# Kernel tuning notes

Hardware: AMD Instinct MI355X
Metric: run time of the kernel (lower is better)

## Reference

```python
import jax, jax.numpy as jnp
import numpy as np

N, L, D, H = 2, 2048, 1024, 16
DK = D // H  # 64


def setup_inputs() -> dict:
    key = jax.random.key(0)
    ks = jax.random.split(key, 8)
    Xq = jax.random.normal(ks[0], (N, L, D), dtype=jnp.float32)
    Xk = jax.random.normal(ks[1], (N, L, D), dtype=jnp.float32)
    Xv = jax.random.normal(ks[2], (N, L, D), dtype=jnp.float32)
    mask_2d = jax.random.randint(ks[3], (N, L, L), 0, 2, dtype=jnp.int32)
    scale = 0.02
    Wq = jax.random.normal(ks[4], (D, D), dtype=jnp.float32) * scale
    Wk = jax.random.normal(ks[5], (D, D), dtype=jnp.float32) * scale
    Wv = jax.random.normal(ks[6], (D, D), dtype=jnp.float32) * scale
    Wo = jax.random.normal(ks[7], (D, D), dtype=jnp.float32) * scale
    return {"Xq": Xq, "Xk": Xk, "Xv": Xv, "Wq": Wq, "Wk": Wk, "Wv": Wv, "Wo": Wo, "mask_2d": mask_2d}


def reference(Xq, Xk, Xv, Wq, Wk, Wv, Wo, mask_2d):
    # Projections (bias=False). Per-head slicing in the original == reshape to [N,L,H,DK].
    Q = (Xq @ Wq).reshape(N, L, H, DK)
    K = (Xk @ Wk).reshape(N, L, H, DK)
    V = (Xv @ Wv).reshape(N, L, H, DK)
    # Scaled dot-product scores: [N, H, L, L]
    scores = jnp.einsum("blhd,bmhd->bhlm", Q, K) / jnp.sqrt(jnp.asarray(DK, scores_dtype(Q)))
    # NOTE: original uses masked_fill(mask==0, 0) BEFORE softmax (zero-fill, not -inf).
    scores = jnp.where(mask_2d[:, None, :, :] == 0, jnp.zeros((), scores.dtype), scores)
    A = jax.nn.softmax(scores, axis=-1)
    O = jnp.einsum("bhlm,bmhd->blhd", A, V).reshape(N, L, D)
    return O @ Wo


def scores_dtype(Q):
    return Q.dtype
```

## Files before the change

kernel.cpp:

```cpp
#include <hip/hip_runtime.h>
#include <hip/hip_bf16.h>

#define NB 2
#define L_SEQ 2048
#define NH 16
#define DKH 64
#define DMODEL 1024
#define MROWS (NB * L_SEQ)
#define QSCALE 0.18033688f

typedef __attribute__((ext_vector_type(8))) short short8;
typedef __attribute__((ext_vector_type(4))) float f32x4;

static __device__ __forceinline__ unsigned short f2bf(float f) {
    unsigned u = __float_as_uint(f);
    u += 0x7fffu + ((u >> 16) & 1u);
    return (unsigned short)(u >> 16);
}

static __device__ __forceinline__ float fexp2(float x) {
#if __has_builtin(__builtin_amdgcn_exp2f)
    return __builtin_amdgcn_exp2f(x);
#else
    return __expf(x * 0.6931471806f);
#endif
}

static __device__ __forceinline__ unsigned pk_bf16(float a, float b) {
    __hip_bfloat162 h = __float22bfloat162_rn(make_float2(a, b));
    return *reinterpret_cast<unsigned*>(&h);
}

static __device__ __forceinline__ void gll16(const void* g, void* l) {
    __builtin_amdgcn_global_load_lds(
        (const __attribute__((address_space(1))) void*)g,
        (__attribute__((address_space(3))) void*)l, 16, 0, 0);
}

__global__ __launch_bounds__(256)
void cast3(const float* __restrict__ s0, const float* __restrict__ s1,
           const float* __restrict__ s2, unsigned short* __restrict__ dst)
{
    const int z = blockIdx.z;
    const float* src = (z == 0) ? s0 : (z == 1) ? s1 : s2;
    const size_t i4 = (size_t)blockIdx.x * 256 + threadIdx.x;
    float4 v = ((const float4*)src)[i4];
    ushort4 o;
    o.x = f2bf(v.x); o.y = f2bf(v.y); o.z = f2bf(v.z); o.w = f2bf(v.w);
    ((ushort4*)(dst + (size_t)z * 4194304))[i4] = o;
}

__global__ __launch_bounds__(256)
void castWt(const float* __restrict__ w0, const float* __restrict__ w1,
            const float* __restrict__ w2, const float* __restrict__ w3,
            unsigned short* __restrict__ dst)
{
    __shared__ float ts[32][33];
    const int z = blockIdx.z;
    const float* W = (z == 0) ? w0 : (z == 1) ? w1 : (z == 2) ? w2 : w3;
    unsigned short* Wt = dst + (size_t)z * 1048576;

    const int k0 = blockIdx.y * 32;
    const int n0 = blockIdx.x * 32;
    const int t  = threadIdx.x;
    const int r  = t >> 3;
    const int c  = (t & 7) * 4;

    float4 v = *(const float4*)&W[(size_t)(k0 + r) * DMODEL + n0 + c];
    ts[r][c + 0] = v.x; ts[r][c + 1] = v.y; ts[r][c + 2] = v.z; ts[r][c + 3] = v.w;
    __syncthreads();

    ushort4 o;
    o.x = f2bf(ts[c + 0][r]); o.y = f2bf(ts[c + 1][r]);
    o.z = f2bf(ts[c + 2][r]); o.w = f2bf(ts[c + 3][r]);
    *(ushort4*)&Wt[(size_t)(n0 + r) * DMODEL + k0 + c] = o;
}

__global__ __launch_bounds__(256)
void maskbits(const int* __restrict__ mask, unsigned long long* __restrict__ MWT)
{
    const int lane = threadIdx.x & 63;
    const size_t wid = (size_t)blockIdx.x * 4 + (threadIdx.x >> 6);
    const int mv = mask[wid * 64 + lane];
    const unsigned long long bits = __ballot(mv != 0);
    if (lane == 0) {
        const int b   = (int)(wid >> 16);
        const int rem = (int)(wid & 65535);
        const int row = rem >> 5;
        const int wd  = rem & 31;
        MWT[((size_t)b * 32 + wd) * L_SEQ + row] = bits;
    }
}

__global__ __launch_bounds__(256)
void gemm_bf16(const unsigned short* __restrict__ Aall,
               const unsigned short* __restrict__ Ball,
               void* __restrict__ Oall,
               const int out_mode, const size_t a_zs, const size_t b_zs,
               const size_t o_zs)
{
    __shared__ __align__(16) unsigned short SMEM[16384];
    unsigned short* As = SMEM;
    unsigned short* Bs = SMEM + 8192;

    const int t    = threadIdx.x;
    const int w    = t >> 6;
    const int lane = t & 63;
    const int z    = blockIdx.z;
    const int m0   = blockIdx.y * 128;
    const int n0   = blockIdx.x * 128;

    const unsigned short* A = Aall + (size_t)z * a_zs;
    const unsigned short* B = Ball + (size_t)z * b_zs;

    const int srow = lane >> 3;
    const int sc   = (lane & 7) ^ srow;

    const unsigned short* ag[4];
    const unsigned short* bg[4];
    unsigned short* la[4];
    unsigned short* lb[4];
#pragma unroll
    for (int j = 0; j < 4; ++j) {
        const int R = w * 32 + j * 8;
        ag[j] = A + (size_t)(m0 + R + srow) * DMODEL + sc * 8;
        bg[j] = B + (size_t)(n0 + R + srow) * DMODEL + sc * 8;
        la[j] = As + R * 64;
        lb[j] = Bs + R * 64;
    }

    const int ml = lane & 15;
    const int q  = lane >> 4;
    const int wm = (w >> 1) * 64;
    const int wn = (w & 1) * 64;

    const f32x4 z4 = {0.f, 0.f, 0.f, 0.f};
    f32x4 acc[4][4];
#pragma unroll
    for (int i = 0; i < 4; ++i)
#pragma unroll
        for (int j = 0; j < 4; ++j) acc[i][j] = z4;

    for (int kt = 0; kt < DMODEL; kt += 64) {
        __syncthreads();
#pragma unroll
        for (int j = 0; j < 4; ++j) {
            gll16(ag[j] + kt, la[j]);
            gll16(bg[j] + kt, lb[j]);
        }
        __syncthreads();

#pragma unroll
        for (int s = 0; s < 2; ++s) {
            short8 av[4], bv[4];
#pragma unroll
            for (int mt = 0; mt < 4; ++mt)
                av[mt] = *(const short8*)
                    &As[(wm + mt * 16 + ml) * 64 + (((s * 4 + q) ^ (ml & 7)) * 8)];
#pragma unroll
            for (int nt = 0; nt < 4; ++nt)
                bv[nt] = *(const short8*)
                    &Bs[(wn + nt * 16 + ml) * 64 + (((s * 4 + q) ^ (ml & 7)) * 8)];
#pragma unroll
            for (int mt = 0; mt < 4; ++mt)
#pragma unroll
                for (int nt = 0; nt < 4; ++nt)
                    acc[mt][nt] = __builtin_amdgcn_mfma_f32_16x16x32_bf16(
                        av[mt], bv[nt], acc[mt][nt], 0, 0, 0);
        }
    }

    if (out_mode == 0) {
        unsigned short* O = (unsigned short*)Oall + (size_t)z * o_zs;
        if (z == 2) {
            __syncthreads();
            unsigned short* Ts = SMEM;
#pragma unroll
            for (int mt = 0; mt < 4; ++mt) {
                const int trow0 = wm + mt * 16 + q * 4;
                const int ch    = trow0 >> 3;
#pragma unroll
                for (int nt = 0; nt < 4; ++nt) {
                    const int tcol = wn + nt * 16 + ml;
                    const int pc   = (ch & 8) | ((ch & 7) ^ (tcol & 7));
                    ushort4 pv;
                    pv.x = f2bf(acc[mt][nt][0]); pv.y = f2bf(acc[mt][nt][1]);
                    pv.z = f2bf(acc[mt][nt][2]); pv.w = f2bf(acc[mt][nt][3]);
                    *(ushort4*)&Ts[tcol * 128 + pc * 8 + (trow0 & 7)] = pv;
                }
            }
            __syncthreads();
            const int bb = m0 >> 11;
            const int l0 = (m0 & (L_SEQ - 1)) + (t & 15) * 8;
            const int cr = t & 15;
#pragma unroll
            for (int it = 0; it < 8; ++it) {
                const int tcol = (t >> 4) + 16 * it;
                const int pc   = (cr & 8) | ((cr & 7) ^ (tcol & 7));
                short8 vv = *(const short8*)&Ts[tcol * 128 + pc * 8];
                const int n  = n0 + tcol;
                const int hh = n >> 6;
                const int dk = n & (DKH - 1);
                *(short8*)&O[((size_t)(bb * NH + hh) * DKH + dk) * L_SEQ + l0] = vv;
            }
        } else {
            const float qs = (z == 0) ? QSCALE : 1.0f;
#pragma unroll
            for (int mt = 0; mt < 4; ++mt) {
                const int gr0 = m0 + wm + mt * 16 + q * 4;
#pragma unroll
                for (int nt = 0; nt < 4; ++nt) {
                    const int col = n0 + wn + nt * 16 + ml;
                    const int hh  = col >> 6;
                    const int dk  = col & (DKH - 1);
#pragma unroll
                    for (int r = 0; r < 4; ++r) {
                        const int row = gr0 + r;
                        const int bb  = row >> 11;
                        const int l   = row & (L_SEQ - 1);
                        O[(((size_t)(bb * NH + hh) * L_SEQ + l) << 6) + dk] =
                            f2bf(acc[mt][nt][r] * qs);
                    }
                }
            }
        }
    } else {
        float* O = (float*)Oall;
#pragma unroll
        for (int mt = 0; mt < 4; ++mt) {
            const int gr0 = m0 + wm + mt * 16 + q * 4;
#pragma unroll
            for (int nt = 0; nt < 4; ++nt) {
                const int col = n0 + wn + nt * 16 + ml;
#pragma unroll
                for (int r = 0; r < 4; ++r)
                    O[(size_t)(gr0 + r) * DMODEL + col] = acc[mt][nt][r];
            }
        }
    }
}

__global__ __launch_bounds__(256, 4)
void attn_mfma(const unsigned short* __restrict__ Qb,
               const unsigned short* __restrict__ Kb,
               const unsigned short* __restrict__ Vtb,
               const unsigned long long* __restrict__ MWT,
               unsigned short* __restrict__ OB)
{
    __shared__ __align__(16) unsigned short Qs[64 * 64];
    __shared__ __align__(16) unsigned short Ks[64 * 64];
    __shared__ __align__(16) unsigned short Vts[64 * 64];
    __shared__ __align__(16) unsigned short Ps[4][16 * 64];
    __shared__ __align__(16) unsigned long long MskL[64];

    const int t    = threadIdx.x;
    const int w    = t >> 6;
    const int lane = t & 63;
    const int ml   = lane & 15;
    const int quad = lane >> 4;

    const int bid = blockIdx.x;
    const int p   = (bid >> 8) * 8 + (bid & 7);
    const int jq  = (bid >> 3) & 31;
    const int h   = p & 15;
    const int b   = p >> 4;
    const int q0  = jq * 64;

    const size_t hoff = (size_t)(b * NH + h) * L_SEQ * DKH;
    const unsigned short* Qh  = Qb  + hoff;
    const unsigned short* Kh  = Kb  + hoff;
    const unsigned short* Vth = Vtb + hoff;

    const int srow = lane >> 3;
    const int sc   = (lane & 7) ^ srow;

    gll16(Qh + (size_t)(q0 + w * 16 + srow) * DKH + sc * 8, &Qs[(w * 16) * 64]);
    gll16(Qh + (size_t)(q0 + w * 16 + 8 + srow) * DKH + sc * 8, &Qs[(w * 16 + 8) * 64]);
    __syncthreads();

    short8 qf[2];
#pragma unroll
    for (int s = 0; s < 2; ++s)
        qf[s] = *(const short8*)
            &Qs[(w * 16 + ml) * 64 + (((s * 4 + quad) ^ (ml & 7)) * 8)];

    const unsigned short* kg0 = Kh + (size_t)(w * 16 + srow) * DKH + sc * 8;
    const unsigned short* kg1 = Kh + (size_t)(w * 16 + 8 + srow) * DKH + sc * 8;
    const unsigned short* vg0 = Vth + (size_t)(w * 16 + srow) * L_SEQ + sc * 8;
    const unsigned short* vg1 = Vth + (size_t)(w * 16 + 8 + srow) * L_SEQ + sc * 8;
    unsigned short* lk0 = &Ks[(w * 16) * 64];
    unsigned short* lk1 = &Ks[(w * 16 + 8) * 64];
    unsigned short* lv0 = &Vts[(w * 16) * 64];
    unsigned short* lv1 = &Vts[(w * 16 + 8) * 64];

    const unsigned long long* mg = MWT + (size_t)b * 32 * L_SEQ + q0 + t;
    unsigned long long m_pf = 0;
    if (t < 64) m_pf = mg[0];

    f32x4 oacc[4];
    const f32x4 z4 = {0.f, 0.f, 0.f, 0.f};
#pragma unroll
    for (int dt = 0; dt < 4; ++dt) oacc[dt] = z4;
    float l_i = 0.f;

    for (int j = 0; j < 32; ++j) {
        __syncthreads();
        gll16(kg0, lk0);  gll16(kg1, lk1);
        gll16(vg0, lv0);  gll16(vg1, lv1);
        kg0 += 64 * DKH;  kg1 += 64 * DKH;
        vg0 += 64;        vg1 += 64;
        if (t < 64) {
            MskL[t] = m_pf;
            if (j < 31) m_pf = mg[(size_t)(j + 1) * L_SEQ];
        }
        __syncthreads();

        f32x4 sacc[4];
#pragma unroll
        for (int kt = 0; kt < 4; ++kt) sacc[kt] = z4;
#pragma unroll
        for (int s = 0; s < 2; ++s) {
            short8 kf[4];
#pragma unroll
            for (int kt = 0; kt < 4; ++kt)
                kf[kt] = *(const short8*)
                    &Ks[(kt * 16 + ml) * 64 + (((s * 4 + quad) ^ (ml & 7)) * 8)];
#pragma unroll
            for (int kt = 0; kt < 4; ++kt)
                sacc[kt] = __builtin_amdgcn_mfma_f32_16x16x32_bf16(
                    kf[kt], qf[s], sacc[kt], 0, 0, 0);
        }

        const unsigned long long wq = MskL[w * 16 + ml] >> (quad * 4);
        const unsigned mlo = (unsigned)wq;
        const unsigned mhi = (unsigned)(wq >> 32);
        float rs = 0.f;
        float pr[4][4];
#pragma unroll
        for (int kt = 0; kt < 4; ++kt) {
            const unsigned word = (kt < 2) ? mlo : mhi;
            const int base = (kt & 1) * 16;
#pragma unroll
            for (int r = 0; r < 4; ++r) {
                const float mf = (float)((word >> (base + r)) & 1u);
                const float e  = fexp2(sacc[kt][r] * mf);
                pr[kt][r] = e;
                rs += e;
            }
        }
        rs += __shfl_xor(rs, 16);
        rs += __shfl_xor(rs, 32);
        l_i += rs;
#pragma unroll
        for (int kt = 0; kt < 4; ++kt) {
            uint2 pk;
            pk.x = pk_bf16(pr[kt][0], pr[kt][1]);
            pk.y = pk_bf16(pr[kt][2], pr[kt][3]);
            const int cp = (kt * 2 + (quad >> 1)) ^ (ml & 7);
            *(uint2*)&Ps[w][ml * 64 + cp * 8 + (quad & 1) * 4] = pk;
        }

#pragma unroll
        for (int s = 0; s < 2; ++s) {
            const short8 pf = *(const short8*)
                &Ps[w][ml * 64 + (((s * 4 + quad) ^ (ml & 7)) * 8)];
#pragma unroll
            for (int dt = 0; dt < 4; ++dt) {
                const short8 vf = *(const short8*)
                    &Vts[(dt * 16 + ml) * 64 + (((s * 4 + quad) ^ (ml & 7)) * 8)];
                oacc[dt] = __builtin_amdgcn_mfma_f32_16x16x32_bf16(
                    vf, pf, oacc[dt], 0, 0, 0);
            }
        }
    }

    const float inv = 1.0f / l_i;
    const int qrow = q0 + w * 16 + ml;
#pragma unroll
    for (int dt = 0; dt < 4; ++dt) {
        ushort4 o4;
        o4.x = f2bf(oacc[dt][0] * inv);
        o4.y = f2bf(oacc[dt][1] * inv);
        o4.z = f2bf(oacc[dt][2] * inv);
        o4.w = f2bf(oacc[dt][3] * inv);
        *(ushort4*)&OB[(size_t)(b * L_SEQ + qrow) * DMODEL + h * DKH +
                       dt * 16 + quad * 4] = o4;
    }
}

extern "C" void kernel_launch(void* const* d_in, const int* in_sizes, int n_in,
                              void* d_out, int out_size, void* d_ws, size_t ws_size,
                              hipStream_t stream)
{
    (void)in_sizes; (void)n_in; (void)out_size; (void)ws_size;

    const float* Xq   = (const float*)d_in[0];
    const float* Xk   = (const float*)d_in[1];
    const float* Xv   = (const float*)d_in[2];
    const float* Wq   = (const float*)d_in[3];
    const float* Wk   = (const float*)d_in[4];
    const float* Wv   = (const float*)d_in[5];
    const float* Wo   = (const float*)d_in[6];
    const int*   mask = (const int*)d_in[7];
    float* out = (float*)d_out;

    char* base = (char*)d_ws;
    unsigned short*     XB  = (unsigned short*)base;
    unsigned short*     WtB = (unsigned short*)(base + (24u << 20));
    unsigned short*     QKV = (unsigned short*)(base + (32u << 20));
    unsigned short*     OB  = (unsigned short*)(base + (56u << 20));
    unsigned long long* MWT = (unsigned long long*)(base + (64u << 20));

    const size_t tsz = (size_t)MROWS * DMODEL;

    cast3<<<dim3(4096, 1, 3), 256, 0, stream>>>(Xq, Xk, Xv, XB);
    castWt<<<dim3(32, 32, 4), 256, 0, stream>>>(Wq, Wk, Wv, Wo, WtB);
    maskbits<<<dim3(32768), 256, 0, stream>>>(mask, MWT);

    gemm_bf16<<<dim3(8, 32, 3), 256, 0, stream>>>(
        XB, WtB, (void*)QKV, 0, tsz, (size_t)DMODEL * DMODEL, tsz);

    attn_mfma<<<dim3(1024), 256, 0, stream>>>(
        QKV, QKV + tsz, QKV + 2 * tsz, MWT, OB);

    gemm_bf16<<<dim3(8, 32, 1), 256, 0, stream>>>(
        OB, WtB + 3 * (size_t)DMODEL * DMODEL, (void*)out, 1, 0, 0, 0);
}
```

Measured before the change: 271.5 us.

## Merge prep kernels, double-buffer GEMM and attention loads, retile output GEMM

```diff
diff --git a/kernel.cpp b/kernel.cpp
--- a/kernel.cpp
+++ b/kernel.cpp
@@ -8,6 +8,7 @@
 #define DMODEL 1024
 #define MROWS (NB * L_SEQ)
 #define QSCALE 0.18033688f
+#define DD (DMODEL * DMODEL)
 
 typedef __attribute__((ext_vector_type(8))) short short8;
 typedef __attribute__((ext_vector_type(4))) float f32x4;
@@ -38,70 +39,64 @@
 }
 
 __global__ __launch_bounds__(256)
-void cast3(const float* __restrict__ s0, const float* __restrict__ s1,
-           const float* __restrict__ s2, unsigned short* __restrict__ dst)
-{
-    const int z = blockIdx.z;
-    const float* src = (z == 0) ? s0 : (z == 1) ? s1 : s2;
-    const size_t i4 = (size_t)blockIdx.x * 256 + threadIdx.x;
-    float4 v = ((const float4*)src)[i4];
-    ushort4 o;
-    o.x = f2bf(v.x); o.y = f2bf(v.y); o.z = f2bf(v.z); o.w = f2bf(v.w);
-    ((ushort4*)(dst + (size_t)z * 4194304))[i4] = o;
-}
-
-__global__ __launch_bounds__(256)
-void castWt(const float* __restrict__ w0, const float* __restrict__ w1,
-            const float* __restrict__ w2, const float* __restrict__ w3,
-            unsigned short* __restrict__ dst)
+void prep(const float* __restrict__ Xq, const float* __restrict__ Xk,
+          const float* __restrict__ Xv, const float* __restrict__ w0,
+          const float* __restrict__ w1, const float* __restrict__ w2,
+          const float* __restrict__ w3, const int* __restrict__ mask,
+          unsigned short* __restrict__ XB, unsigned short* __restrict__ WtB,
+          unsigned long long* __restrict__ MWT)
 {
     __shared__ float ts[32][33];
-    const int z = blockIdx.z;
-    const float* W = (z == 0) ? w0 : (z == 1) ? w1 : (z == 2) ? w2 : w3;
-    unsigned short* Wt = dst + (size_t)z * 1048576;
-
-    const int k0 = blockIdx.y * 32;
-    const int n0 = blockIdx.x * 32;
+    const int bx = blockIdx.x;
     const int t  = threadIdx.x;
-    const int r  = t >> 3;
-    const int c  = (t & 7) * 4;
-
-    float4 v = *(const float4*)&W[(size_t)(k0 + r) * DMODEL + n0 + c];
-    ts[r][c + 0] = v.x; ts[r][c + 1] = v.y; ts[r][c + 2] = v.z; ts[r][c + 3] = v.w;
-    __syncthreads();
-
-    ushort4 o;
-    o.x = f2bf(ts[c + 0][r]); o.y = f2bf(ts[c + 1][r]);
-    o.z = f2bf(ts[c + 2][r]); o.w = f2bf(ts[c + 3][r]);
-    *(ushort4*)&Wt[(size_t)(n0 + r) * DMODEL + k0 + c] = o;
+
+    if (bx < 12288) {
+        const int z = bx >> 12;
+        const float* src = (z == 0) ? Xq : (z == 1) ? Xk : Xv;
+        const size_t i4 = (size_t)(bx & 4095) * 256 + t;
+        float4 v = ((const float4*)src)[i4];
+        ushort4 o;
+        o.x = f2bf(v.x); o.y = f2bf(v.y); o.z = f2bf(v.z); o.w = f2bf(v.w);
+        ((ushort4*)(XB + (size_t)z * 4194304))[i4] = o;
+    } else if (bx < 16384) {
+        const int idx = bx - 12288;
+        const int z   = idx >> 10;
+        const int rem = idx & 1023;
+        const float* W = (z == 0) ? w0 : (z == 1) ? w1 : (z == 2) ? w2 : w3;
+        unsigned short* Wt = WtB + (size_t)z * DD;
+        const int n0 = (rem & 31) * 32;
+        const int k0 = (rem >> 5) * 32;
+        const int r  = t >> 3;
+        const int c  = (t & 7) * 4;
+        float4 v = *(const float4*)&W[(size_t)(k0 + r) * DMODEL + n0 + c];
+        ts[r][c + 0] = v.x; ts[r][c + 1] = v.y;
+        ts[r][c + 2] = v.z; ts[r][c + 3] = v.w;
+        __syncthreads();
+        ushort4 o;
+        o.x = f2bf(ts[c + 0][r]); o.y = f2bf(ts[c + 1][r]);
+        o.z = f2bf(ts[c + 2][r]); o.w = f2bf(ts[c + 3][r]);
+        *(ushort4*)&Wt[(size_t)(n0 + r) * DMODEL + k0 + c] = o;
+    } else {
+        const int lane = t & 63;
+        const size_t wid = (size_t)(bx - 16384) * 4 + (t >> 6);
+        const int mv = mask[wid * 64 + lane];
+        const unsigned long long bits = __ballot(mv != 0);
+        if (lane == 0) {
+            const int b   = (int)(wid >> 16);
+            const int rem = (int)(wid & 65535);
+            const int row = rem >> 5;
+            const int wd  = rem & 31;
+            MWT[((size_t)b * 32 + wd) * L_SEQ + row] = bits;
+        }
+    }
 }
 
 __global__ __launch_bounds__(256)
-void maskbits(const int* __restrict__ mask, unsigned long long* __restrict__ MWT)
-{
-    const int lane = threadIdx.x & 63;
-    const size_t wid = (size_t)blockIdx.x * 4 + (threadIdx.x >> 6);
-    const int mv = mask[wid * 64 + lane];
-    const unsigned long long bits = __ballot(mv != 0);
-    if (lane == 0) {
-        const int b   = (int)(wid >> 16);
-        const int rem = (int)(wid & 65535);
-        const int row = rem >> 5;
-        const int wd  = rem & 31;
-        MWT[((size_t)b * 32 + wd) * L_SEQ + row] = bits;
-    }
-}
-
-__global__ __launch_bounds__(256)
-void gemm_bf16(const unsigned short* __restrict__ Aall,
-               const unsigned short* __restrict__ Ball,
-               void* __restrict__ Oall,
-               const int out_mode, const size_t a_zs, const size_t b_zs,
-               const size_t o_zs)
+void gemm_qkv(const unsigned short* __restrict__ XB,
+              const unsigned short* __restrict__ WtB,
+              unsigned short* __restrict__ QKV)
 {
     __shared__ __align__(16) unsigned short SMEM[16384];
-    unsigned short* As = SMEM;
-    unsigned short* Bs = SMEM + 8192;
 
     const int t    = threadIdx.x;
     const int w    = t >> 6;
@@ -110,23 +105,22 @@
     const int m0   = blockIdx.y * 128;
     const int n0   = blockIdx.x * 128;
 
-    const unsigned short* A = Aall + (size_t)z * a_zs;
-    const unsigned short* B = Ball + (size_t)z * b_zs;
-
-    const int srow = lane >> 3;
-    const int sc   = (lane & 7) ^ srow;
-
-    const unsigned short* ag[4];
-    const unsigned short* bg[4];
-    unsigned short* la[4];
-    unsigned short* lb[4];
-#pragma unroll
-    for (int j = 0; j < 4; ++j) {
-        const int R = w * 32 + j * 8;
-        ag[j] = A + (size_t)(m0 + R + srow) * DMODEL + sc * 8;
-        bg[j] = B + (size_t)(n0 + R + srow) * DMODEL + sc * 8;
-        la[j] = As + R * 64;
-        lb[j] = Bs + R * 64;
+    const unsigned short* A = XB  + (size_t)z * ((size_t)MROWS * DMODEL);
+    const unsigned short* B = WtB + (size_t)z * DD;
+
+    const int srow = lane >> 2;
+    const int sc4  = (lane & 3) ^ (srow & 3);
+
+    const unsigned short* ag[2];
+    const unsigned short* bg[2];
+    int lao[2], lbo[2];
+#pragma unroll
+    for (int g = 0; g < 2; ++g) {
+        const int R = w * 32 + g * 16;
+        ag[g] = A + (size_t)(m0 + R + srow) * DMODEL + sc4 * 8;
+        bg[g] = B + (size_t)(n0 + R + srow) * DMODEL + sc4 * 8;
+        lao[g] = R * 32;
+        lbo[g] = R * 32;
     }
 
     const int ml = lane & 15;
@@ -141,101 +135,179 @@
 #pragma unroll
         for (int j = 0; j < 4; ++j) acc[i][j] = z4;
 
-    for (int kt = 0; kt < DMODEL; kt += 64) {
-        __syncthreads();
-#pragma unroll
-        for (int j = 0; j < 4; ++j) {
-            gll16(ag[j] + kt, la[j]);
-            gll16(bg[j] + kt, lb[j]);
-        }
-        __syncthreads();
-
-#pragma unroll
-        for (int s = 0; s < 2; ++s) {
-            short8 av[4], bv[4];
-#pragma unroll
-            for (int mt = 0; mt < 4; ++mt)
-                av[mt] = *(const short8*)
-                    &As[(wm + mt * 16 + ml) * 64 + (((s * 4 + q) ^ (ml & 7)) * 8)];
+#pragma unroll
+    for (int g = 0; g < 2; ++g) {
+        gll16(ag[g], &SMEM[lao[g]]);
+        gll16(bg[g], &SMEM[8192 + lbo[g]]);
+    }
+
+    for (int j = 0; j < 32; ++j) {
+        const int cur = j & 1;
+        __syncthreads();
+        if (j < 31) {
+            const int kt = (j + 1) * 32;
+            const int nb = (cur ^ 1) * 4096;
+#pragma unroll
+            for (int g = 0; g < 2; ++g) {
+                gll16(ag[g] + kt, &SMEM[nb + lao[g]]);
+                gll16(bg[g] + kt, &SMEM[8192 + nb + lbo[g]]);
+            }
+        }
+        const unsigned short* As = &SMEM[cur * 4096];
+        const unsigned short* Bs = &SMEM[8192 + cur * 4096];
+        short8 av[4], bv[4];
+#pragma unroll
+        for (int mt = 0; mt < 4; ++mt)
+            av[mt] = *(const short8*)
+                &As[(wm + mt * 16 + ml) * 32 + ((q ^ (ml & 3)) * 8)];
+#pragma unroll
+        for (int nt = 0; nt < 4; ++nt)
+            bv[nt] = *(const short8*)
+                &Bs[(wn + nt * 16 + ml) * 32 + ((q ^ (ml & 3)) * 8)];
+#pragma unroll
+        for (int mt = 0; mt < 4; ++mt)
 #pragma unroll
             for (int nt = 0; nt < 4; ++nt)
-                bv[nt] = *(const short8*)
-                    &Bs[(wn + nt * 16 + ml) * 64 + (((s * 4 + q) ^ (ml & 7)) * 8)];
-#pragma unroll
-            for (int mt = 0; mt < 4; ++mt)
-#pragma unroll
-                for (int nt = 0; nt < 4; ++nt)
-                    acc[mt][nt] = __builtin_amdgcn_mfma_f32_16x16x32_bf16(
-                        av[mt], bv[nt], acc[mt][nt], 0, 0, 0);
-        }
-    }
-
-    if (out_mode == 0) {
-        unsigned short* O = (unsigned short*)Oall + (size_t)z * o_zs;
-        if (z == 2) {
-            __syncthreads();
-            unsigned short* Ts = SMEM;
-#pragma unroll
-            for (int mt = 0; mt < 4; ++mt) {
-                const int trow0 = wm + mt * 16 + q * 4;
-                const int ch    = trow0 >> 3;
-#pragma unroll
-                for (int nt = 0; nt < 4; ++nt) {
-                    const int tcol = wn + nt * 16 + ml;
-                    const int pc   = (ch & 8) | ((ch & 7) ^ (tcol & 7));
-                    ushort4 pv;
-                    pv.x = f2bf(acc[mt][nt][0]); pv.y = f2bf(acc[mt][nt][1]);
-                    pv.z = f2bf(acc[mt][nt][2]); pv.w = f2bf(acc[mt][nt][3]);
-                    *(ushort4*)&Ts[tcol * 128 + pc * 8 + (trow0 & 7)] = pv;
+                acc[mt][nt] = __builtin_amdgcn_mfma_f32_16x16x32_bf16(
+                    av[mt], bv[nt], acc[mt][nt], 0, 0, 0);
+    }
+
+    unsigned short* O = QKV + (size_t)z * ((size_t)MROWS * DMODEL);
+    if (z == 2) {
+        __syncthreads();
+        unsigned short* Ts = SMEM;
+#pragma unroll
+        for (int mt = 0; mt < 4; ++mt) {
+            const int trow0 = wm + mt * 16 + q * 4;
+            const int ch    = trow0 >> 3;
+#pragma unroll
+            for (int nt = 0; nt < 4; ++nt) {
+                const int tcol = wn + nt * 16 + ml;
+                const int pc   = (ch & 8) | ((ch & 7) ^ (tcol & 7));
+                ushort4 pv;
+                pv.x = f2bf(acc[mt][nt][0]); pv.y = f2bf(acc[mt][nt][1]);
+                pv.z = f2bf(acc[mt][nt][2]); pv.w = f2bf(acc[mt][nt][3]);
+                *(ushort4*)&Ts[tcol * 128 + pc * 8 + (trow0 & 7)] = pv;
+            }
+        }
+        __syncthreads();
+        const int bb = m0 >> 11;
+        const int l0 = (m0 & (L_SEQ - 1)) + (t & 15) * 8;
+        const int cr = t & 15;
+#pragma unroll
+        for (int it = 0; it < 8; ++it) {
+            const int tcol = (t >> 4) + 16 * it;
+            const int pc   = (cr & 8) | ((cr & 7) ^ (tcol & 7));
+            short8 vv = *(const short8*)&Ts[tcol * 128 + pc * 8];
+            const int n  = n0 + tcol;
+            const int hh = n >> 6;
+            const int dk = n & (DKH - 1);
+            *(short8*)&O[((size_t)(bb * NH + hh) * DKH + dk) * L_SEQ + l0] = vv;
+        }
+    } else {
+        const float qs = (z == 0) ? QSCALE : 1.0f;
+#pragma unroll
+        for (int mt = 0; mt < 4; ++mt) {
+            const int gr0 = m0 + wm + mt * 16 + q * 4;
+#pragma unroll
+            for (int nt = 0; nt < 4; ++nt) {
+                const int col = n0 + wn + nt * 16 + ml;
+                const int hh  = col >> 6;
+                const int dk  = col & (DKH - 1);
+#pragma unroll
+                for (int r = 0; r < 4; ++r) {
+                    const int row = gr0 + r;
+                    const int bb  = row >> 11;
+                    const int l   = row & (L_SEQ - 1);
+                    O[(((size_t)(bb * NH + hh) * L_SEQ + l) << 6) + dk] =
+                        f2bf(acc[mt][nt][r] * qs);
                 }
             }
-            __syncthreads();
-            const int bb = m0 >> 11;
-            const int l0 = (m0 & (L_SEQ - 1)) + (t & 15) * 8;
-            const int cr = t & 15;
-#pragma unroll
-            for (int it = 0; it < 8; ++it) {
-                const int tcol = (t >> 4) + 16 * it;
-                const int pc   = (cr & 8) | ((cr & 7) ^ (tcol & 7));
-                short8 vv = *(const short8*)&Ts[tcol * 128 + pc * 8];
-                const int n  = n0 + tcol;
-                const int hh = n >> 6;
-                const int dk = n & (DKH - 1);
-                *(short8*)&O[((size_t)(bb * NH + hh) * DKH + dk) * L_SEQ + l0] = vv;
-            }
-        } else {
-            const float qs = (z == 0) ? QSCALE : 1.0f;
-#pragma unroll
-            for (int mt = 0; mt < 4; ++mt) {
-                const int gr0 = m0 + wm + mt * 16 + q * 4;
-#pragma unroll
-                for (int nt = 0; nt < 4; ++nt) {
-                    const int col = n0 + wn + nt * 16 + ml;
-                    const int hh  = col >> 6;
-                    const int dk  = col & (DKH - 1);
-#pragma unroll
-                    for (int r = 0; r < 4; ++r) {
-                        const int row = gr0 + r;
-                        const int bb  = row >> 11;
-                        const int l   = row & (L_SEQ - 1);
-                        O[(((size_t)(bb * NH + hh) * L_SEQ + l) << 6) + dk] =
-                            f2bf(acc[mt][nt][r] * qs);
-                    }
-                }
-            }
-        }
-    } else {
-        float* O = (float*)Oall;
-#pragma unroll
-        for (int mt = 0; mt < 4; ++mt) {
-            const int gr0 = m0 + wm + mt * 16 + q * 4;
-#pragma unroll
-            for (int nt = 0; nt < 4; ++nt) {
-                const int col = n0 + wn + nt * 16 + ml;
-#pragma unroll
-                for (int r = 0; r < 4; ++r)
-                    O[(size_t)(gr0 + r) * DMODEL + col] = acc[mt][nt][r];
-            }
+        }
+    }
+}
+
+__global__ __launch_bounds__(256)
+void gemm_out(const unsigned short* __restrict__ OB,
+              const unsigned short* __restrict__ Wt,
+              float* __restrict__ out)
+{
+    __shared__ __align__(16) unsigned short As[2][2048];
+    __shared__ __align__(16) unsigned short Bs[2][4096];
+
+    const int t    = threadIdx.x;
+    const int w    = t >> 6;
+    const int lane = t & 63;
+    const int m0   = blockIdx.y * 64;
+    const int n0   = blockIdx.x * 128;
+
+    const int srow = lane >> 2;
+    const int sc4  = (lane & 3) ^ (srow & 3);
+
+    const unsigned short* ag =
+        OB + (size_t)(m0 + w * 16 + srow) * DMODEL + sc4 * 8;
+    const unsigned short* bg[2];
+    int lbo[2];
+#pragma unroll
+    for (int g = 0; g < 2; ++g) {
+        const int R = w * 32 + g * 16;
+        bg[g] = Wt + (size_t)(n0 + R + srow) * DMODEL + sc4 * 8;
+        lbo[g] = R * 32;
+    }
+    const int lao = (w * 16) * 32;
+
+    const int ml = lane & 15;
+    const int q  = lane >> 4;
+    const int wm = (w >> 1) * 32;
+    const int wn = (w & 1) * 64;
+
+    const f32x4 z4 = {0.f, 0.f, 0.f, 0.f};
+    f32x4 acc[2][4];
+#pragma unroll
+    for (int i = 0; i < 2; ++i)
+#pragma unroll
+        for (int j = 0; j < 4; ++j) acc[i][j] = z4;
+
+    gll16(ag, &As[0][lao]);
+#pragma unroll
+    for (int g = 0; g < 2; ++g) gll16(bg[g], &Bs[0][lbo[g]]);
+
+    for (int j = 0; j < 32; ++j) {
+        const int cur = j & 1;
+        __syncthreads();
+        if (j < 31) {
+            const int kt = (j + 1) * 32;
+            gll16(ag + kt, &As[cur ^ 1][lao]);
+#pragma unroll
+            for (int g = 0; g < 2; ++g)
+                gll16(bg[g] + kt, &Bs[cur ^ 1][lbo[g]]);
+        }
+        short8 av[2], bv[4];
+#pragma unroll
+        for (int mt = 0; mt < 2; ++mt)
+            av[mt] = *(const short8*)
+                &As[cur][(wm + mt * 16 + ml) * 32 + ((q ^ (ml & 3)) * 8)];
+#pragma unroll
+        for (int nt = 0; nt < 4; ++nt)
+            bv[nt] = *(const short8*)
+                &Bs[cur][(wn + nt * 16 + ml) * 32 + ((q ^ (ml & 3)) * 8)];
+#pragma unroll
+        for (int mt = 0; mt < 2; ++mt)
+#pragma unroll
+            for (int nt = 0; nt < 4; ++nt)
+                acc[mt][nt] = __builtin_amdgcn_mfma_f32_16x16x32_bf16(
+                    av[mt], bv[nt], acc[mt][nt], 0, 0, 0);
+    }
+
+#pragma unroll
+    for (int mt = 0; mt < 2; ++mt) {
+        const int gr0 = m0 + wm + mt * 16 + q * 4;
+#pragma unroll
+        for (int nt = 0; nt < 4; ++nt) {
+            const int col = n0 + wn + nt * 16 + ml;
+#pragma unroll
+            for (int r = 0; r < 4; ++r)
+                out[(size_t)(gr0 + r) * DMODEL + col] = acc[mt][nt][r];
         }
     }
 }
@@ -247,11 +319,9 @@
                const unsigned long long* __restrict__ MWT,
                unsigned short* __restrict__ OB)
 {
-    __shared__ __align__(16) unsigned short Qs[64 * 64];
-    __shared__ __align__(16) unsigned short Ks[64 * 64];
-    __shared__ __align__(16) unsigned short Vts[64 * 64];
-    __shared__ __align__(16) unsigned short Ps[4][16 * 64];
-    __shared__ __align__(16) unsigned long long MskL[64];
+    __shared__ __align__(16) unsigned short Ks[2][4096];
+    __shared__ __align__(16) unsigned short Vts[2][4096];
+    __shared__ __align__(16) unsigned short Ps[4][1024];
 
     const int t    = threadIdx.x;
     const int w    = t >> 6;
@@ -271,31 +341,25 @@
     const unsigned short* Kh  = Kb  + hoff;
     const unsigned short* Vth = Vtb + hoff;
 
+    short8 qf[2];
+#pragma unroll
+    for (int s = 0; s < 2; ++s)
+        qf[s] = *(const short8*)
+            &Qh[(size_t)(q0 + w * 16 + ml) * DKH + (s * 4 + quad) * 8];
+
     const int srow = lane >> 3;
     const int sc   = (lane & 7) ^ srow;
-
-    gll16(Qh + (size_t)(q0 + w * 16 + srow) * DKH + sc * 8, &Qs[(w * 16) * 64]);
-    gll16(Qh + (size_t)(q0 + w * 16 + 8 + srow) * DKH + sc * 8, &Qs[(w * 16 + 8) * 64]);
-    __syncthreads();
-
-    short8 qf[2];
-#pragma unroll
-    for (int s = 0; s < 2; ++s)
-        qf[s] = *(const short8*)
-            &Qs[(w * 16 + ml) * 64 + (((s * 4 + quad) ^ (ml & 7)) * 8)];
 
     const unsigned short* kg0 = Kh + (size_t)(w * 16 + srow) * DKH + sc * 8;
     const unsigned short* kg1 = Kh + (size_t)(w * 16 + 8 + srow) * DKH + sc * 8;
     const unsigned short* vg0 = Vth + (size_t)(w * 16 + srow) * L_SEQ + sc * 8;
     const unsigned short* vg1 = Vth + (size_t)(w * 16 + 8 + srow) * L_SEQ + sc * 8;
-    unsigned short* lk0 = &Ks[(w * 16) * 64];
-    unsigned short* lk1 = &Ks[(w * 16 + 8) * 64];
-    unsigned short* lv0 = &Vts[(w * 16) * 64];
-    unsigned short* lv1 = &Vts[(w * 16 + 8) * 64];
-
-    const unsigned long long* mg = MWT + (size_t)b * 32 * L_SEQ + q0 + t;
-    unsigned long long m_pf = 0;
-    if (t < 64) m_pf = mg[0];
+    const int lk0 = (w * 16) * 64;
+    const int lk1 = (w * 16 + 8) * 64;
+
+    const unsigned long long* mg_w = MWT + (size_t)b * 32 * L_SEQ + q0 + w * 16;
+    unsigned long long mcur = 0, mnxt = 0;
+    if (lane < 16) mcur = mg_w[lane];
 
     f32x4 oacc[4];
     const f32x4 z4 = {0.f, 0.f, 0.f, 0.f};
@@ -303,17 +367,20 @@
     for (int dt = 0; dt < 4; ++dt) oacc[dt] = z4;
     float l_i = 0.f;
 
+    gll16(kg0, &Ks[0][lk0]);  gll16(kg1, &Ks[0][lk1]);
+    gll16(vg0, &Vts[0][lk0]); gll16(vg1, &Vts[0][lk1]);
+    kg0 += 64 * DKH; kg1 += 64 * DKH; vg0 += 64; vg1 += 64;
+
     for (int j = 0; j < 32; ++j) {
-        __syncthreads();
-        gll16(kg0, lk0);  gll16(kg1, lk1);
-        gll16(vg0, lv0);  gll16(vg1, lv1);
-        kg0 += 64 * DKH;  kg1 += 64 * DKH;
-        vg0 += 64;        vg1 += 64;
-        if (t < 64) {
-            MskL[t] = m_pf;
-            if (j < 31) m_pf = mg[(size_t)(j + 1) * L_SEQ];
-        }
-        __syncthreads();
+        const int cur = j & 1;
+        __syncthreads();
+        if (j < 31) {
+            const int nxt = cur ^ 1;
+            gll16(kg0, &Ks[nxt][lk0]);  gll16(kg1, &Ks[nxt][lk1]);
+            gll16(vg0, &Vts[nxt][lk0]); gll16(vg1, &Vts[nxt][lk1]);
+            kg0 += 64 * DKH; kg1 += 64 * DKH; vg0 += 64; vg1 += 64;
+            if (lane < 16) mnxt = mg_w[(size_t)(j + 1) * L_SEQ + lane];
+        }
 
         f32x4 sacc[4];
 #pragma unroll
@@ -324,14 +391,14 @@
 #pragma unroll
             for (int kt = 0; kt < 4; ++kt)
                 kf[kt] = *(const short8*)
-                    &Ks[(kt * 16 + ml) * 64 + (((s * 4 + quad) ^ (ml & 7)) * 8)];
+                    &Ks[cur][(kt * 16 + ml) * 64 + (((s * 4 + quad) ^ (ml & 7)) * 8)];
 #pragma unroll
             for (int kt = 0; kt < 4; ++kt)
                 sacc[kt] = __builtin_amdgcn_mfma_f32_16x16x32_bf16(
                     kf[kt], qf[s], sacc[kt], 0, 0, 0);
         }
 
-        const unsigned long long wq = MskL[w * 16 + ml] >> (quad * 4);
+        const unsigned long long wq = __shfl(mcur, ml) >> (quad * 4);
         const unsigned mlo = (unsigned)wq;
         const unsigned mhi = (unsigned)(wq >> 32);
         float rs = 0.f;
@@ -367,11 +434,12 @@
 #pragma unroll
             for (int dt = 0; dt < 4; ++dt) {
                 const short8 vf = *(const short8*)
-                    &Vts[(dt * 16 + ml) * 64 + (((s * 4 + quad) ^ (ml & 7)) * 8)];
+                    &Vts[cur][(dt * 16 + ml) * 64 + (((s * 4 + quad) ^ (ml & 7)) * 8)];
                 oacc[dt] = __builtin_amdgcn_mfma_f32_16x16x32_bf16(
                     vf, pf, oacc[dt], 0, 0, 0);
             }
         }
+        mcur = mnxt;
     }
 
     const float inv = 1.0f / l_i;
@@ -413,16 +481,13 @@
 
     const size_t tsz = (size_t)MROWS * DMODEL;
 
-    cast3<<<dim3(4096, 1, 3), 256, 0, stream>>>(Xq, Xk, Xv, XB);
-    castWt<<<dim3(32, 32, 4), 256, 0, stream>>>(Wq, Wk, Wv, Wo, WtB);
-    maskbits<<<dim3(32768), 256, 0, stream>>>(mask, MWT);
-
-    gemm_bf16<<<dim3(8, 32, 3), 256, 0, stream>>>(
-        XB, WtB, (void*)QKV, 0, tsz, (size_t)DMODEL * DMODEL, tsz);
+    prep<<<dim3(49152), 256, 0, stream>>>(
+        Xq, Xk, Xv, Wq, Wk, Wv, Wo, mask, XB, WtB, MWT);
+
+    gemm_qkv<<<dim3(8, 32, 3), 256, 0, stream>>>(XB, WtB, QKV);
 
     attn_mfma<<<dim3(1024), 256, 0, stream>>>(
         QKV, QKV + tsz, QKV + 2 * tsz, MWT, OB);
 
-    gemm_bf16<<<dim3(8, 32, 1), 256, 0, stream>>>(
-        OB, WtB + 3 * (size_t)DMODEL * DMODEL, (void*)out, 1, 0, 0, 0);
-}
+    gemm_out<<<dim3(8, 64), 256, 0, stream>>>(OB, WtB + 3 * (size_t)DD, out);
+}
```

After: 273.1 us. About the same (+0.6%).
